# Performance work log

Hardware: AMD Instinct MI355X
Metric: run time of the kernel (lower is better)

## Reference

```python
import jax, jax.numpy as jnp
import numpy as np

N = 32        # fixed segment-tree span in the original module
LEVELS = 5    # log2(N) descent steps (l<r loop runs exactly 5 times)
B, S, D = 16, 8192, 64


def _prefix(x):
    # P[b, m] = sum_{l=1}^{m} x[b, l]  (leaf l holds x[l]; x[0] is never used)
    return jnp.concatenate([jnp.zeros_like(x[:, :1]), jnp.cumsum(x[:, 1:N], axis=1)], axis=1)


def _seg(P, a, b, n, bidx):
    # sum of leaves l in [a, b] with l < n, via prefix sums; shapes a,b,n: [B,S]
    hi = jnp.minimum(b, n - 1)
    ok = hi >= a
    hic = jnp.clip(hi, 0, N - 1)
    v = P[bidx, hic] - P[bidx, a - 1]          # [B,S,D]
    return jnp.where(ok[..., None], v, jnp.zeros((), P.dtype))


def reference(queries, keys, values, valid_lens):
    b, s, d = queries.shape
    if valid_lens is None:
        n = jnp.full((b, s), keys.shape[1], jnp.int32)
    elif valid_lens.ndim == 1:
        n = jnp.broadcast_to(valid_lens.astype(jnp.int32)[:, None], (b, s))
    else:
        n = valid_lens.astype(jnp.int32)
    Pk = _prefix(keys)    # [B,N,D]
    Pv = _prefix(values)  # [B,N,D]
    bidx = jnp.arange(b)[:, None]
    l = jnp.ones((b, s), jnp.int32)
    r = jnp.full((b, s), N, jnp.int32)
    ans = jnp.zeros((b, s, d), queries.dtype)
    for _ in range(LEVELS):
        mid = (l + r) >> 1
        kL = _seg(Pk, l, mid, n, bidx)
        kR = _seg(Pk, mid + 1, r, n, bidx)
        ls = jax.nn.sigmoid(jnp.sum(queries * kL, axis=-1))  # [B,S]
        rs = jax.nn.sigmoid(jnp.sum(queries * kR, axis=-1))
        cond = ls >= rs
        vL = _seg(Pv, l, mid, n, bidx)
        vR = _seg(Pv, mid + 1, r, n, bidx)
        add = jnp.where(cond[..., None], vR * rs[..., None], vL * ls[..., None])
        ans = ans * 0.5 + add
        r = jnp.where(cond, mid, r)
        l = jnp.where(cond, l, mid + 1)
    return ans


def setup_inputs() -> dict:
    key = jax.random.key(0)
    k1, k2, k3, k4 = jax.random.split(key, 4)
    return {
        "queries": jax.random.normal(k1, (B, S, D), jnp.float32),
        "keys": jax.random.normal(k2, (B, N, D), jnp.float32),
        "values": jax.random.normal(k3, (B, N, D), jnp.float32),
        "valid_lens": jax.random.randint(k4, (B,), 0, 32, jnp.int64),
    }
```

## Files before the change

kernel.cpp:

```cpp
#include <hip/hip_runtime.h>
#include <math.h>


#define SEG_N   32
#define DIM     64
#define LEVELS  5
#define QPB     64
#define THREADS 256
#define PAD     68

#define DPP_QUAD_XOR1   0xB1
#define DPP_QUAD_XOR2   0x4E
#define DPP_ROW_HMIRROR 0x141

template <int CTRL>
__device__ __forceinline__ float dpp_xadd(float v) {
    const int s = __builtin_amdgcn_update_dpp(0, __float_as_int(v), CTRL, 0xf, 0xf, true);
    return v + __int_as_float(s);
}

__device__ __forceinline__ float group8_sum(float v) {
    v = dpp_xadd<DPP_QUAD_XOR1>(v);
    v = dpp_xadd<DPP_QUAD_XOR2>(v);
    v = dpp_xadd<DPP_ROW_HMIRROR>(v);
    return v;
}

__device__ __forceinline__ float4 f4sub(const float4 a, const float4 b) {
    return make_float4(a.x - b.x, a.y - b.y, a.z - b.z, a.w - b.w);
}
__device__ __forceinline__ float4 sel4(bool c, const float4 a, const float4 b) {
    return make_float4(c ? a.x : b.x, c ? a.y : b.y, c ? a.z : b.z, c ? a.w : b.w);
}
__device__ __forceinline__ float dot4(const float4 a, const float4 b) {
    return a.x * b.x + a.y * b.y + a.z * b.z + a.w * b.w;
}
__device__ __forceinline__ void fma4(float4& acc, const float4 hi, const float4 lo, float w) {
    acc.x = fmaf(hi.x - lo.x, w, acc.x);
    acc.y = fmaf(hi.y - lo.y, w, acc.y);
    acc.z = fmaf(hi.z - lo.z, w, acc.z);
    acc.w = fmaf(hi.w - lo.w, w, acc.w);
}

__global__ __launch_bounds__(THREADS) void segtree_attn_kernel(
    const float* __restrict__ q,
    const float* __restrict__ keys,
    const float* __restrict__ values,
    const int*   __restrict__ vlen,
    float*       __restrict__ out,
    int S)
{
    __shared__ float Pk[SEG_N * PAD];
    __shared__ float Pv[SEG_N * PAD];

    const int b = blockIdx.y;
    const int t = threadIdx.x;

    if (t < 2 * DIM) {
        const int col = t & (DIM - 1);
        const float* src = ((t < DIM) ? keys : values) + (size_t)b * SEG_N * DIM + col;
        float* dst = (t < DIM) ? Pk : Pv;
        float acc = 0.0f;
        dst[col] = 0.0f;
        #pragma unroll
        for (int row = 1; row < SEG_N; ++row) {
            acc += src[row * DIM];
            dst[row * PAD + col] = acc;
        }
    }
    const int n = vlen[b];
    __syncthreads();

    const int g = t >> 3;
    const int u = t & 7;
    const int c = u * 8;

    const int hnc = max(min(n - 1, SEG_N - 1), 0);
    const float4 pkN0 = *(const float4*)&Pk[hnc * PAD + c];
    const float4 pkN1 = *(const float4*)&Pk[hnc * PAD + c + 4];

    const int sA = blockIdx.x * QPB + g;
    const int sB = sA + 32;
    const float scale[LEVELS] = {0.0625f, 0.125f, 0.25f, 0.5f, 1.0f};

    const float* qpA = q + ((size_t)b * S + sA) * DIM + c;
    const float* qpB = q + ((size_t)b * S + sB) * DIM + c;
    const float4 qA0 = *(const float4*)qpA;
    const float4 qA1 = *(const float4*)(qpA + 4);
    const float4 qB0 = *(const float4*)qpB;
    const float4 qB1 = *(const float4*)(qpB + 4);

    int lA = 1, rA = SEG_N, rowA_A = 0, rowR_A = hnc;
    int lB = 1, rB = SEG_N, rowA_B = 0, rowR_B = hnc;
    float4 pkA_A0 = make_float4(0.f,0.f,0.f,0.f), pkA_A1 = make_float4(0.f,0.f,0.f,0.f);
    float4 pkA_B0 = make_float4(0.f,0.f,0.f,0.f), pkA_B1 = make_float4(0.f,0.f,0.f,0.f);
    float4 pkR_A0 = pkN0, pkR_A1 = pkN1;
    float4 pkR_B0 = pkN0, pkR_B1 = pkN1;

    float wA[LEVELS], wB[LEVELS];
    int   rows[LEVELS];

    #pragma unroll
    for (int lev = 0; lev < LEVELS; ++lev) {
        const int midA = (lA + rA) >> 1;
        const int midB = (lB + rB) >> 1;

        const float4 pkM_A0 = *(const float4*)&Pk[midA * PAD + c];
        const float4 pkM_A1 = *(const float4*)&Pk[midA * PAD + c + 4];
        const float4 pkM_B0 = *(const float4*)&Pk[midB * PAD + c];
        const float4 pkM_B1 = *(const float4*)&Pk[midB * PAD + c + 4];

        const bool inLA = (midA <= n - 1);
        const bool inLB = (midB <= n - 1);
        const int rowHiL_A = inLA ? midA : hnc;
        const int rowHiL_B = inLB ? midB : hnc;
        const float4 pkHiL_A0 = sel4(inLA, pkM_A0, pkN0);
        const float4 pkHiL_A1 = sel4(inLA, pkM_A1, pkN1);
        const float4 pkHiL_B0 = sel4(inLB, pkM_B0, pkN0);
        const float4 pkHiL_B1 = sel4(inLB, pkM_B1, pkN1);

        float dLA = dot4(qA0, f4sub(pkHiL_A0, pkA_A0)) + dot4(qA1, f4sub(pkHiL_A1, pkA_A1));
        float dRA = dot4(qA0, f4sub(pkR_A0,  pkM_A0)) + dot4(qA1, f4sub(pkR_A1,  pkM_A1));
        float dLB = dot4(qB0, f4sub(pkHiL_B0, pkA_B0)) + dot4(qB1, f4sub(pkHiL_B1, pkA_B1));
        float dRB = dot4(qB0, f4sub(pkR_B0,  pkM_B0)) + dot4(qB1, f4sub(pkR_B1,  pkM_B1));

        dLA = group8_sum(dLA);
        dRA = group8_sum(dRA);
        dLB = group8_sum(dLB);
        dRB = group8_sum(dRB);

        const bool okLA = (min(midA, n - 1) >= lA);
        const bool okRA = (min(rA,   n - 1) >= midA + 1);
        const bool okLB = (min(midB, n - 1) >= lB);
        const bool okRB = (min(rB,   n - 1) >= midB + 1);

        const float sLA = okLA ? dLA : 0.0f;
        const float sRA = okRA ? dRA : 0.0f;
        const float sLB = okLB ? dLB : 0.0f;
        const float sRB = okRB ? dRB : 0.0f;

        const float lsA = 1.0f / (1.0f + __expf(-sLA));
        const float rsA = 1.0f / (1.0f + __expf(-sRA));
        const float lsB = 1.0f / (1.0f + __expf(-sLB));
        const float rsB = 1.0f / (1.0f + __expf(-sRB));

        const bool condA = (lsA >= rsA);
        const bool condB = (lsB >= rsB);

        const bool  okselA = condA ? okRA : okLA;
        const bool  okselB = condB ? okRB : okLB;
        const float wselA  = condA ? rsA : lsA;
        const float wselB  = condB ? rsB : lsB;
        wA[lev] = okselA ? (wselA * scale[lev]) : 0.0f;
        wB[lev] = okselB ? (wselB * scale[lev]) : 0.0f;

        const int hiA = condA ? rowR_A : rowHiL_A;
        const int loA = condA ? midA   : rowA_A;
        const int hiB = condB ? rowR_B : rowHiL_B;
        const int loB = condB ? midB   : rowA_B;
        rows[lev] = hiA | (loA << 8) | (hiB << 16) | (loB << 24);

        if (condA) {
            rA = midA; rowR_A = rowHiL_A;
            pkR_A0 = pkHiL_A0; pkR_A1 = pkHiL_A1;
        } else {
            lA = midA + 1; rowA_A = midA;
            pkA_A0 = pkM_A0; pkA_A1 = pkM_A1;
        }
        if (condB) {
            rB = midB; rowR_B = rowHiL_B;
            pkR_B0 = pkHiL_B0; pkR_B1 = pkHiL_B1;
        } else {
            lB = midB + 1; rowA_B = midB;
            pkA_B0 = pkM_B0; pkA_B1 = pkM_B1;
        }
    }

    float4 aA0 = make_float4(0.f,0.f,0.f,0.f), aA1 = make_float4(0.f,0.f,0.f,0.f);
    float4 aB0 = make_float4(0.f,0.f,0.f,0.f), aB1 = make_float4(0.f,0.f,0.f,0.f);
    #pragma unroll
    for (int lev = 0; lev < LEVELS; ++lev) {
        const int pk = rows[lev];
        const int hiAr = pk & 0xFF, loAr = (pk >> 8) & 0xFF;
        const int hiBr = (pk >> 16) & 0xFF, loBr = (pk >> 24) & 0xFF;
        const float4 hA0 = *(const float4*)&Pv[hiAr * PAD + c];
        const float4 hA1 = *(const float4*)&Pv[hiAr * PAD + c + 4];
        const float4 lA0 = *(const float4*)&Pv[loAr * PAD + c];
        const float4 lA1 = *(const float4*)&Pv[loAr * PAD + c + 4];
        fma4(aA0, hA0, lA0, wA[lev]);
        fma4(aA1, hA1, lA1, wA[lev]);
        const float4 hB0 = *(const float4*)&Pv[hiBr * PAD + c];
        const float4 hB1 = *(const float4*)&Pv[hiBr * PAD + c + 4];
        const float4 lB0 = *(const float4*)&Pv[loBr * PAD + c];
        const float4 lB1 = *(const float4*)&Pv[loBr * PAD + c + 4];
        fma4(aB0, hB0, lB0, wB[lev]);
        fma4(aB1, hB1, lB1, wB[lev]);
    }

    float* opA = out + ((size_t)b * S + sA) * DIM + c;
    float* opB = out + ((size_t)b * S + sB) * DIM + c;
    *(float4*)opA       = aA0;
    *(float4*)(opA + 4) = aA1;
    *(float4*)opB       = aB0;
    *(float4*)(opB + 4) = aB1;
}

extern "C" void kernel_launch(void* const* d_in, const int* in_sizes, int n_in,
                              void* d_out, int out_size, void* d_ws, size_t ws_size,
                              hipStream_t stream) {
    const float* q    = (const float*)d_in[0];
    const float* keys = (const float*)d_in[1];
    const float* vals = (const float*)d_in[2];
    const int*   vl   = (const int*)d_in[3];
    float* out = (float*)d_out;

    const int B = in_sizes[3];
    const int S = in_sizes[0] / (B * DIM);

    dim3 grid(S / QPB, B);
    segtree_attn_kernel<<<grid, THREADS, 0, stream>>>(q, keys, vals, vl, out, S);
}
```

Baseline: 26.53 us.

## Speculatively prefetch both child midpoints and hoist query loads before prefix build

Each level now loads the prefix rows for both possible next midpoints (mid-step and mid+step, clamped to the valid length) before the comparison resolves, then picks one with a select. This takes the LDS load latency off the serial decision chain. Midpoint rows are pre-clamped to hnc, which removes the per-level inLA/sel4 logic. Query global loads are moved ahead of the shared-memory prefix construction so they overlap it. The cost is twice the LDS reads per level and more live registers.

Measured after the change: 26.81 us. No clear change (+1.1%).

```diff
diff --git a/kernel.cpp b/kernel.cpp
--- a/kernel.cpp
+++ b/kernel.cpp
@@ -55,6 +55,19 @@
 
     const int b = blockIdx.y;
     const int t = threadIdx.x;
+    const int g = t >> 3;
+    const int u = t & 7;
+    const int c = u * 8;
+
+    const int sA = blockIdx.x * QPB + g;
+    const int sB = sA + 32;
+
+    const float* qpA = q + ((size_t)b * S + sA) * DIM + c;
+    const float* qpB = q + ((size_t)b * S + sB) * DIM + c;
+    const float4 qA0 = *(const float4*)qpA;
+    const float4 qA1 = *(const float4*)(qpA + 4);
+    const float4 qB0 = *(const float4*)qpB;
+    const float4 qB1 = *(const float4*)(qpB + 4);
 
     if (t < 2 * DIM) {
         const int col = t & (DIM - 1);
@@ -71,58 +84,55 @@
     const int n = vlen[b];
     __syncthreads();
 
-    const int g = t >> 3;
-    const int u = t & 7;
-    const int c = u * 8;
-
     const int hnc = max(min(n - 1, SEG_N - 1), 0);
-    const float4 pkN0 = *(const float4*)&Pk[hnc * PAD + c];
-    const float4 pkN1 = *(const float4*)&Pk[hnc * PAD + c + 4];
-
-    const int sA = blockIdx.x * QPB + g;
-    const int sB = sA + 32;
     const float scale[LEVELS] = {0.0625f, 0.125f, 0.25f, 0.5f, 1.0f};
 
-    const float* qpA = q + ((size_t)b * S + sA) * DIM + c;
-    const float* qpB = q + ((size_t)b * S + sB) * DIM + c;
-    const float4 qA0 = *(const float4*)qpA;
-    const float4 qA1 = *(const float4*)(qpA + 4);
-    const float4 qB0 = *(const float4*)qpB;
-    const float4 qB1 = *(const float4*)(qpB + 4);
-
+    const int cm16 = min(16, hnc);
+    float4 pkM_A0 = *(const float4*)&Pk[cm16 * PAD + c];
+    float4 pkM_A1 = *(const float4*)&Pk[cm16 * PAD + c + 4];
+    float4 pkM_B0 = pkM_A0, pkM_B1 = pkM_A1;
+    const float4 pkRi0 = *(const float4*)&Pk[hnc * PAD + c];
+    const float4 pkRi1 = *(const float4*)&Pk[hnc * PAD + c + 4];
+
+    float4 pkR_A0 = pkRi0, pkR_A1 = pkRi1;
+    float4 pkR_B0 = pkRi0, pkR_B1 = pkRi1;
+    float4 pkA_A0 = make_float4(0.f,0.f,0.f,0.f), pkA_A1 = make_float4(0.f,0.f,0.f,0.f);
+    float4 pkA_B0 = make_float4(0.f,0.f,0.f,0.f), pkA_B1 = make_float4(0.f,0.f,0.f,0.f);
+
+    int midA = 16, midB = 16;
     int lA = 1, rA = SEG_N, rowA_A = 0, rowR_A = hnc;
     int lB = 1, rB = SEG_N, rowA_B = 0, rowR_B = hnc;
-    float4 pkA_A0 = make_float4(0.f,0.f,0.f,0.f), pkA_A1 = make_float4(0.f,0.f,0.f,0.f);
-    float4 pkA_B0 = make_float4(0.f,0.f,0.f,0.f), pkA_B1 = make_float4(0.f,0.f,0.f,0.f);
-    float4 pkR_A0 = pkN0, pkR_A1 = pkN1;
-    float4 pkR_B0 = pkN0, pkR_B1 = pkN1;
 
     float wA[LEVELS], wB[LEVELS];
     int   rows[LEVELS];
 
     #pragma unroll
     for (int lev = 0; lev < LEVELS; ++lev) {
-        const int midA = (lA + rA) >> 1;
-        const int midB = (lB + rB) >> 1;
-
-        const float4 pkM_A0 = *(const float4*)&Pk[midA * PAD + c];
-        const float4 pkM_A1 = *(const float4*)&Pk[midA * PAD + c + 4];
-        const float4 pkM_B0 = *(const float4*)&Pk[midB * PAD + c];
-        const float4 pkM_B1 = *(const float4*)&Pk[midB * PAD + c + 4];
-
-        const bool inLA = (midA <= n - 1);
-        const bool inLB = (midB <= n - 1);
-        const int rowHiL_A = inLA ? midA : hnc;
-        const int rowHiL_B = inLB ? midB : hnc;
-        const float4 pkHiL_A0 = sel4(inLA, pkM_A0, pkN0);
-        const float4 pkHiL_A1 = sel4(inLA, pkM_A1, pkN1);
-        const float4 pkHiL_B0 = sel4(inLB, pkM_B0, pkN0);
-        const float4 pkHiL_B1 = sel4(inLB, pkM_B1, pkN1);
-
-        float dLA = dot4(qA0, f4sub(pkHiL_A0, pkA_A0)) + dot4(qA1, f4sub(pkHiL_A1, pkA_A1));
-        float dRA = dot4(qA0, f4sub(pkR_A0,  pkM_A0)) + dot4(qA1, f4sub(pkR_A1,  pkM_A1));
-        float dLB = dot4(qB0, f4sub(pkHiL_B0, pkA_B0)) + dot4(qB1, f4sub(pkHiL_B1, pkA_B1));
-        float dRB = dot4(qB0, f4sub(pkR_B0,  pkM_B0)) + dot4(qB1, f4sub(pkR_B1,  pkM_B1));
+        const int step = 8 >> lev;
+        const int cmA = min(midA, hnc);
+        const int cmB = min(midB, hnc);
+
+        float4 sLoA0, sLoA1, sHiA0, sHiA1, sLoB0, sLoB1, sHiB0, sHiB1;
+        int midLoA = 0, midHiA = 0, midLoB = 0, midHiB = 0;
+        if (lev < LEVELS - 1) {
+            midLoA = midA - step; midHiA = midA + step;
+            midLoB = midB - step; midHiB = midB + step;
+            const int rLoA = min(midLoA, hnc), rHiA = min(midHiA, hnc);
+            const int rLoB = min(midLoB, hnc), rHiB = min(midHiB, hnc);
+            sLoA0 = *(const float4*)&Pk[rLoA * PAD + c];
+            sLoA1 = *(const float4*)&Pk[rLoA * PAD + c + 4];
+            sHiA0 = *(const float4*)&Pk[rHiA * PAD + c];
+            sHiA1 = *(const float4*)&Pk[rHiA * PAD + c + 4];
+            sLoB0 = *(const float4*)&Pk[rLoB * PAD + c];
+            sLoB1 = *(const float4*)&Pk[rLoB * PAD + c + 4];
+            sHiB0 = *(const float4*)&Pk[rHiB * PAD + c];
+            sHiB1 = *(const float4*)&Pk[rHiB * PAD + c + 4];
+        }
+
+        float dLA = dot4(qA0, f4sub(pkM_A0, pkA_A0)) + dot4(qA1, f4sub(pkM_A1, pkA_A1));
+        float dRA = dot4(qA0, f4sub(pkR_A0, pkM_A0)) + dot4(qA1, f4sub(pkR_A1, pkM_A1));
+        float dLB = dot4(qB0, f4sub(pkM_B0, pkA_B0)) + dot4(qB1, f4sub(pkM_B1, pkA_B1));
+        float dRB = dot4(qB0, f4sub(pkR_B0, pkM_B0)) + dot4(qB1, f4sub(pkR_B1, pkM_B1));
 
         dLA = group8_sum(dLA);
         dRA = group8_sum(dRA);
@@ -154,25 +164,34 @@
         wA[lev] = okselA ? (wselA * scale[lev]) : 0.0f;
         wB[lev] = okselB ? (wselB * scale[lev]) : 0.0f;
 
-        const int hiA = condA ? rowR_A : rowHiL_A;
+        const int hiA = condA ? rowR_A : cmA;
         const int loA = condA ? midA   : rowA_A;
-        const int hiB = condB ? rowR_B : rowHiL_B;
+        const int hiB = condB ? rowR_B : cmB;
         const int loB = condB ? midB   : rowA_B;
         rows[lev] = hiA | (loA << 8) | (hiB << 16) | (loB << 24);
 
         if (condA) {
-            rA = midA; rowR_A = rowHiL_A;
-            pkR_A0 = pkHiL_A0; pkR_A1 = pkHiL_A1;
+            rA = midA; rowR_A = cmA;
+            pkR_A0 = pkM_A0; pkR_A1 = pkM_A1;
         } else {
             lA = midA + 1; rowA_A = midA;
             pkA_A0 = pkM_A0; pkA_A1 = pkM_A1;
         }
         if (condB) {
-            rB = midB; rowR_B = rowHiL_B;
-            pkR_B0 = pkHiL_B0; pkR_B1 = pkHiL_B1;
+            rB = midB; rowR_B = cmB;
+            pkR_B0 = pkM_B0; pkR_B1 = pkM_B1;
         } else {
             lB = midB + 1; rowA_B = midB;
             pkA_B0 = pkM_B0; pkA_B1 = pkM_B1;
+        }
+
+        if (lev < LEVELS - 1) {
+            midA = condA ? midLoA : midHiA;
+            midB = condB ? midLoB : midHiB;
+            pkM_A0 = sel4(condA, sLoA0, sHiA0);
+            pkM_A1 = sel4(condA, sLoA1, sHiA1);
+            pkM_B0 = sel4(condB, sLoB0, sHiB0);
+            pkM_B1 = sel4(condB, sLoB1, sHiB1);
         }
     }
 
```
